# Performance work log

Hardware: AMD Instinct MI355X
Metric: run time of the kernel (lower is better)

Reference implementation:

```python
import jax, jax.numpy as jnp
import numpy as np
from jax import lax

T, B, XD, AD, H, OUT = 200, 1024, 48, 15, 512, 32
IN = XD + AD + 1  # 64


def _uniform(key, shape, scale):
    return jax.random.uniform(key, shape, jnp.float32, -scale, scale)


def setup_inputs() -> dict:
    key = jax.random.key(0)
    ks = jax.random.split(key, 16)
    k_lstm = 1.0 / np.sqrt(H)
    k1 = 1.0 / np.sqrt(H)
    k2 = 1.0 / np.sqrt(H + 1)
    return {
        "x": jax.random.normal(ks[0], (T, B, XD), jnp.float32),
        "a": jax.random.normal(ks[1], (T, B, AD), jnp.float32),
        "m": jax.random.uniform(ks[2], (T, B, 1), jnp.float32),
        # LSTM params (torch gate order: i, f, g, o)
        "w_ih": _uniform(ks[3], (4 * H, IN), k_lstm),
        "w_hh": _uniform(ks[4], (4 * H, H), k_lstm),
        "b_ih": _uniform(ks[5], (4 * H,), k_lstm),
        "b_hh": _uniform(ks[6], (4 * H,), k_lstm),
        # lin head: Linear(H, H+1) -> tanh -> Linear(H+1, OUT) -> tanh
        "lw1": _uniform(ks[7], (H + 1, H), k1),
        "lb1": _uniform(ks[8], (H + 1,), k1),
        "lw2": _uniform(ks[9], (OUT, H + 1), k2),
        "lb2": _uniform(ks[10], (OUT,), k2),
        # log_var head (same structure)
        "vw1": _uniform(ks[11], (H + 1, H), k1),
        "vb1": _uniform(ks[12], (H + 1,), k1),
        "vw2": _uniform(ks[13], (OUT, H + 1), k2),
        "vb2": _uniform(ks[14], (OUT,), k2),
    }


def _lstm(x_in, w_ih, w_hh, b_ih, b_hh):
    # x_in: [T, B, IN]; single-layer LSTM, zero initial state (torch default)
    b = x_in.shape[1]
    h0 = jnp.zeros((b, H), x_in.dtype)
    c0 = jnp.zeros((b, H), x_in.dtype)

    def step(carry, xt):
        h, c = carry
        gates = xt @ w_ih.T + b_ih + h @ w_hh.T + b_hh  # [B, 4H]
        i, f, g, o = jnp.split(gates, 4, axis=-1)
        c = jax.nn.sigmoid(f) * c + jax.nn.sigmoid(i) * jnp.tanh(g)
        h = jax.nn.sigmoid(o) * jnp.tanh(c)
        return (h, c), h

    _, hs = lax.scan(step, (h0, c0), x_in)
    return hs  # [T, B, H]


def _mlp(h, w1, b1, w2, b2):
    return jnp.tanh(jnp.tanh(h @ w1.T + b1) @ w2.T + b2)


def reference(x, a, m, w_ih, w_hh, b_ih, b_hh, lw1, lb1, lw2, lb2, vw1, vb1, vw2, vb2):
    # reverse=True
    x = jnp.flip(x, 0)
    a = jnp.flip(a, 0)
    m = jnp.flip(m, 0)
    t_steps = m.shape[0]
    t = jnp.arange(t_steps, dtype=x.dtype)[:, None, None] / jnp.max(m)  # [T,1,1]
    t = jnp.broadcast_to(t, (t_steps, m.shape[1], 1))
    x_in = jnp.concatenate([x, a, t], axis=-1)  # [T, B, IN]
    hs = _lstm(x_in, w_ih, w_hh, b_ih, b_hh)
    h_last = hs[-1]  # [B, H] (output_all=False)
    mu = _mlp(h_last, lw1, lb1, lw2, lb2)
    log_var = _mlp(h_last, vw1, vb1, vw2, vb2)
    return mu, log_var
```

## Files before the change

kernel.cpp:

```cpp
#include <hip/hip_runtime.h>
#include <cstdint>


typedef _Float16 f16;
typedef __attribute__((ext_vector_type(8))) _Float16 f16x8;
typedef __attribute__((ext_vector_type(8))) unsigned short u16x8;
typedef __attribute__((ext_vector_type(4))) float f32x4;

#define DEV __device__ __forceinline__

DEV float sigf(float x) { return 1.0f / (1.0f + expf(-x)); }

__global__ void __launch_bounds__(256)
wprep_kernel(const float* __restrict__ w_ih, const float* __restrict__ w_hh,
             uint4* __restrict__ wsw, unsigned* __restrict__ bar) {
  int idx = blockIdx.x * 256 + threadIdx.x;
  if (blockIdx.x == 0 && threadIdx.x < 256) bar[threadIdx.x] = 0u;
  if (idx >= 16 * 9 * 32 * 64) return;
  int jt = idx / 18432, rem = idx - jt * 18432;
  int ch = rem >> 11, r2 = rem & 2047;
  int Lb = r2 >> 6, lane = r2 & 63;
  int p = Lb & 1, ks = (Lb >> 1) & 1, jg = (Lb >> 2) & 1, g = Lb >> 3;
  int n = g * 512 + jt * 32 + jg * 16 + (lane & 15);
  int kb = ch * 64 + ks * 32 + (lane >> 4) * 8;
  f16x8 o;
#pragma unroll
  for (int e = 0; e < 8; e++) {
    int k = kb + e;
    float v = (k < 64) ? w_ih[n * 64 + k] : w_hh[(size_t)n * 512 + (k - 64)];
    f16 hi = (f16)v;
    o[e] = p ? (f16)(v - (float)hi) : hi;
  }
  wsw[idx] = *(uint4*)&o;
}

__global__ void __launch_bounds__(512, 2)
lstm_persist(const float* __restrict__ x, const float* __restrict__ a,
             const uint4* __restrict__ wsw,
             const float* __restrict__ b_ih, const float* __restrict__ b_hh,
             unsigned* __restrict__ hpk, float* __restrict__ h_final,
             const float* __restrict__ maxm_p, unsigned* __restrict__ bar) {
  __shared__ unsigned short sAB[2][24576];

  const int tid = threadIdx.x;
  const int lane = tid & 63;
  const int w = tid >> 6;
  const int rg = w >> 1, jg = w & 1;
  const int bid = blockIdx.x;
  const int mt = bid >> 4, jt = bid & 15;
  const int m0 = mt * 64;
  const int jjcol = jt * 32 + jg * 16 + (lane & 15);

  float bias[4];
#pragma unroll
  for (int g = 0; g < 4; g++)
    bias[g] = b_ih[g * 512 + jjcol] + b_hh[g * 512 + jjcol];
  f32x4 cc = {0.f, 0.f, 0.f, 0.f};
  const float mxm = *maxm_p;

  const int a_ln = tid & 63;
  const int a_La2 = tid >> 6;
  const int a_rg2 = a_La2 >> 1, a_ks2 = a_La2 & 1;
  const size_t a_off = (size_t)(m0 + a_rg2 * 16 + (a_ln & 15)) * 512 +
                       a_ks2 * 32 + (a_ln >> 4) * 8;

  for (int s = 0; s < 200; s++) {
    const int nch = (s == 0) ? 1 : 9;
    const int bin = s & 1;
    const unsigned* hin = hpk + (size_t)bin * 1024 * 512;
    unsigned* hout = hpk + (size_t)(bin ^ 1) * 1024 * 512;

    {
#pragma unroll
      for (int i = 0; i < 4; i++) {
        int id = tid + i * 512;
        uint4 v = wsw[(size_t)(jt * 9 + 0) * 2048 + id];
        *(uint4*)&sAB[0][8192 + id * 8] = v;
      }
      const float ts = (float)s / mxm;
      size_t srow = (size_t)(199 - s) * 1024 + m0;
      int row = tid >> 3, k8 = (tid & 7) * 8;
      float v[8];
#pragma unroll
      for (int e = 0; e < 8; e++) {
        int k = k8 + e;
        if (k < 48)      v[e] = x[(srow + row) * 48 + k];
        else if (k < 63) v[e] = a[(srow + row) * 15 + (k - 48)];
        else             v[e] = ts;
      }
      f16x8 hi, lo;
#pragma unroll
      for (int e = 0; e < 8; e++) {
        f16 h8 = (f16)v[e];
        hi[e] = h8; lo[e] = (f16)(v[e] - (float)h8);
      }
      int rg2 = row >> 4, ks2 = k8 >> 5;
      int ln = (((k8 & 31) >> 3) << 4) | (row & 15);
      int Lhi = (rg2 * 2 + ks2) * 2;
      *(f16x8*)&sAB[0][(Lhi * 64 + ln) * 8] = hi;
      *(f16x8*)&sAB[0][((Lhi + 1) * 64 + ln) * 8] = lo;
    }
    __syncthreads();

    f32x4 acc[4];
#pragma unroll
    for (int g = 0; g < 4; g++) acc[g] = (f32x4){0.f, 0.f, 0.f, 0.f};

    int cur = 0;
    for (int ch = 0; ch < nch; ch++) {
      const bool pref = (ch + 1 < nch);
      unsigned long long pa[4];
      uint4 pb[4];
      if (pref) {
        const unsigned* src = hin + a_off + ch * 64;
#pragma unroll
        for (int j = 0; j < 4; j++)
          pa[j] = __hip_atomic_load((const unsigned long long*)src + j,
                                    __ATOMIC_RELAXED, __HIP_MEMORY_SCOPE_AGENT);
#pragma unroll
        for (int i = 0; i < 4; i++)
          pb[i] = wsw[(size_t)(jt * 9 + ch + 1) * 2048 + tid + i * 512];
      }

      const unsigned short* buf = sAB[cur];
#pragma unroll
      for (int ks = 0; ks < 2; ks++) {
        f16x8 Ah = *(const f16x8*)&buf[(((rg * 2 + ks) * 2 + 0) * 64 + lane) * 8];
        f16x8 Al = *(const f16x8*)&buf[(((rg * 2 + ks) * 2 + 1) * 64 + lane) * 8];
        f16x8 Bh[4], Bl[4];
#pragma unroll
        for (int g = 0; g < 4; g++) {
          int base = 8192 + ((((g * 2 + jg) * 2 + ks) * 2) * 64 + lane) * 8;
          Bh[g] = *(const f16x8*)&buf[base];
          Bl[g] = *(const f16x8*)&buf[base + 512];
        }
        __builtin_amdgcn_s_setprio(1);
#pragma unroll
        for (int g = 0; g < 4; g++)
          acc[g] = __builtin_amdgcn_mfma_f32_16x16x32_f16(Ah, Bh[g], acc[g], 0, 0, 0);
#pragma unroll
        for (int g = 0; g < 4; g++)
          acc[g] = __builtin_amdgcn_mfma_f32_16x16x32_f16(Al, Bh[g], acc[g], 0, 0, 0);
#pragma unroll
        for (int g = 0; g < 4; g++)
          acc[g] = __builtin_amdgcn_mfma_f32_16x16x32_f16(Ah, Bl[g], acc[g], 0, 0, 0);
        __builtin_amdgcn_s_setprio(0);
      }

      if (pref) {
        unsigned short* nb = sAB[cur ^ 1];
        u16x8 HI, LO;
#pragma unroll
        for (int e = 0; e < 8; e++) {
          unsigned int u = (unsigned int)(pa[e >> 1] >> ((e & 1) * 32));
          HI[e] = (unsigned short)(u & 0xffffu);
          LO[e] = (unsigned short)(u >> 16);
        }
        int Lhi = a_La2 * 2;
        *(u16x8*)&nb[(Lhi * 64 + a_ln) * 8] = HI;
        *(u16x8*)&nb[((Lhi + 1) * 64 + a_ln) * 8] = LO;
#pragma unroll
        for (int i = 0; i < 4; i++)
          *(uint4*)&nb[8192 + (tid + i * 512) * 8] = pb[i];
      }
      __syncthreads();
      cur ^= 1;
    }

#pragma unroll
    for (int i = 0; i < 4; i++) {
      float gi = acc[0][i] + bias[0];
      float gf = acc[1][i] + bias[1];
      float gg = acc[2][i] + bias[2];
      float go = acc[3][i] + bias[3];
      float c = sigf(gf) * cc[i] + sigf(gi) * tanhf(gg);
      cc[i] = c;
      float h = sigf(go) * tanhf(c);
      size_t r = (size_t)(m0 + rg * 16 + (lane >> 4) * 4 + i) * 512 + jjcol;
      f16 h8 = (f16)h;
      f16 l8 = (f16)(h - (float)h8);
      unsigned pk = ((unsigned)__builtin_bit_cast(unsigned short, l8) << 16) |
                    (unsigned)__builtin_bit_cast(unsigned short, h8);
      __hip_atomic_store(&hout[r], pk, __ATOMIC_RELAXED, __HIP_MEMORY_SCOPE_AGENT);
      if (s == 199) h_final[r] = h;
    }

    __syncthreads();
    if (tid == 0) {
      __hip_atomic_fetch_add(&bar[mt * 16], 1u,
                             __ATOMIC_RELAXED, __HIP_MEMORY_SCOPE_AGENT);
      unsigned target = 16u * (unsigned)(s + 1);
      while (__hip_atomic_load(&bar[mt * 16], __ATOMIC_RELAXED,
                               __HIP_MEMORY_SCOPE_AGENT) < target)
        __builtin_amdgcn_s_sleep(2);
    }
    __syncthreads();
  }
}

__global__ void __launch_bounds__(1024)
maxm_kernel(const float* __restrict__ mv, float* __restrict__ out) {
  __shared__ float red[1024];
  int tid = threadIdx.x;
  float mx = -3.0e38f;
  for (int i = tid; i < 200 * 1024; i += 1024) mx = fmaxf(mx, mv[i]);
  red[tid] = mx;
  __syncthreads();
  for (int s = 512; s > 0; s >>= 1) {
    if (tid < s) red[tid] = fmaxf(red[tid], red[tid + s]);
    __syncthreads();
  }
  if (tid == 0) *out = red[0];
}

__global__ void __launch_bounds__(256, 2)
head1_valu(const float* __restrict__ h, const float* __restrict__ lw1,
           const float* __restrict__ lb1, const float* __restrict__ vw1,
           const float* __restrict__ vb1, float* __restrict__ z) {
  __shared__ float sAT[64 * 68];
  const int tid = threadIdx.x;
  const int rg = tid & 15;
  const int cgrp = tid >> 4;
  const int bid = blockIdx.x;
  const int mt = bid & 15, nt = bid >> 4;
  const int m0 = mt * 64;
  const int nb = nt * 64 + cgrp * 4;

  const float* wr[4];
  float bias[4];
  int hdv[4], wnv[4], valid[4];
#pragma unroll
  for (int c = 0; c < 4; c++) {
    int n = nb + c;
    valid[c] = (n < 1026);
    int hd = valid[c] ? (n >= 513) : 0;
    int wn = valid[c] ? (n - hd * 513) : 0;
    hdv[c] = hd; wnv[c] = wn;
    wr[c] = (hd ? vw1 : lw1) + (size_t)wn * 512;
    bias[c] = valid[c] ? (hd ? vb1[wn] : lb1[wn]) : 0.f;
  }

  float acc[4][4];
#pragma unroll
  for (int i = 0; i < 4; i++)
#pragma unroll
    for (int c = 0; c < 4; c++) acc[i][c] = 0.f;

  for (int ch = 0; ch < 8; ch++) {
    int k0 = ch * 64;
    for (int idx = tid; idx < 4096; idx += 256) {
      int row = idx >> 6, k = idx & 63;
      sAT[k * 68 + row] = h[(size_t)(m0 + row) * 512 + k0 + k];
    }
    __syncthreads();
#pragma unroll 4
    for (int k4 = 0; k4 < 16; k4++) {
      f32x4 wv[4];
#pragma unroll
      for (int c = 0; c < 4; c++)
        wv[c] = *(const f32x4*)(wr[c] + k0 + k4 * 4);
      f32x4 rv[4];
#pragma unroll
      for (int kk = 0; kk < 4; kk++)
        rv[kk] = *(const f32x4*)&sAT[(k4 * 4 + kk) * 68 + rg * 4];
#pragma unroll
      for (int kk = 0; kk < 4; kk++)
#pragma unroll
        for (int c = 0; c < 4; c++) {
          acc[0][c] += rv[kk][0] * wv[c][kk];
          acc[1][c] += rv[kk][1] * wv[c][kk];
          acc[2][c] += rv[kk][2] * wv[c][kk];
          acc[3][c] += rv[kk][3] * wv[c][kk];
        }
    }
    __syncthreads();
  }
#pragma unroll
  for (int c = 0; c < 4; c++) {
    if (!valid[c]) continue;
#pragma unroll
    for (int i = 0; i < 4; i++) {
      int m = m0 + rg * 4 + i;
      z[(size_t)hdv[c] * 1024 * 520 + (size_t)m * 520 + wnv[c]] =
          tanhf(acc[i][c] + bias[c]);
    }
  }
}

__global__ void __launch_bounds__(256)
head2_valu(const float* __restrict__ z, const float* __restrict__ lw2,
           const float* __restrict__ lb2, const float* __restrict__ vw2,
           const float* __restrict__ vb2, float* __restrict__ out) {
  __shared__ float sZ[8 * 133];
  __shared__ float sW[32 * 133];
  const int tid = threadIdx.x;
  const int bid = blockIdx.x;
  const int gr0 = bid * 8;
  const int hd = gr0 >> 10;
  const int b0 = gr0 & 1023;
  const float* w2 = hd ? vw2 : lw2;
  const float* b2 = hd ? vb2 : lb2;
  const float* zh = z + (size_t)hd * 1024 * 520;
  const int rloc = tid >> 5, col = tid & 31;
  float acc = 0.f;

  for (int ch = 0; ch < 5; ch++) {
    int kc = ch * 128;
    for (int idx = tid; idx < 1024; idx += 256) {
      int row = idx >> 7, k = idx & 127;
      int kk = kc + k;
      sZ[row * 133 + k] = (kk < 513) ? zh[(size_t)(b0 + row) * 520 + kk] : 0.f;
    }
    for (int idx = tid; idx < 4096; idx += 256) {
      int row = idx >> 7, k = idx & 127;
      int kk = kc + k;
      sW[row * 133 + k] = (kk < 513) ? w2[(size_t)row * 513 + kk] : 0.f;
    }
    __syncthreads();
#pragma unroll 8
    for (int k = 0; k < 128; k++)
      acc += sZ[rloc * 133 + k] * sW[col * 133 + k];
    __syncthreads();
  }
  out[(size_t)hd * 32768 + (size_t)(b0 + rloc) * 32 + col] = tanhf(acc + b2[col]);
}

extern "C" void kernel_launch(void* const* d_in, const int* in_sizes, int n_in,
                              void* d_out, int out_size, void* d_ws, size_t ws_size,
                              hipStream_t stream) {
  (void)in_sizes; (void)n_in; (void)out_size; (void)ws_size;
  const float* x    = (const float*)d_in[0];
  const float* a    = (const float*)d_in[1];
  const float* mm   = (const float*)d_in[2];
  const float* w_ih = (const float*)d_in[3];
  const float* w_hh = (const float*)d_in[4];
  const float* b_ih = (const float*)d_in[5];
  const float* b_hh = (const float*)d_in[6];
  const float* lw1  = (const float*)d_in[7];
  const float* lb1  = (const float*)d_in[8];
  const float* lw2  = (const float*)d_in[9];
  const float* lb2  = (const float*)d_in[10];
  const float* vw1  = (const float*)d_in[11];
  const float* vb1  = (const float*)d_in[12];
  const float* vw2  = (const float*)d_in[13];
  const float* vb2  = (const float*)d_in[14];

  char* wsb = (char*)d_ws;
  float*    maxm  = (float*)wsb;
  unsigned* bar   = (unsigned*)(wsb + 256);
  float*    z     = (float*)(wsb + 4096);
  float*    h_fin = (float*)(wsb + 4263936);
  uint4*    wsw   = (uint4*)(wsb + 6361088);
  unsigned* hpk   = (unsigned*)(wsb + 11079680);

  maxm_kernel<<<1, 1024, 0, stream>>>(mm, maxm);
  wprep_kernel<<<1152, 256, 0, stream>>>(w_ih, w_hh, wsw, bar);

  {
    const float* xa = x; const float* aa = a;
    const uint4* wswa = wsw;
    const float* biha = b_ih; const float* bhha = b_hh;
    unsigned* hpka = hpk;
    float* hfa = h_fin; const float* mxa = maxm;
    unsigned* bara = bar;
    void* kargs[] = {&xa, &aa, &wswa, &biha, &bhha,
                     &hpka, &hfa, &mxa, &bara};
    hipLaunchCooperativeKernel((void*)lstm_persist, dim3(256), dim3(512),
                               kargs, 0, stream);
  }

  head1_valu<<<272, 256, 0, stream>>>(h_fin, lw1, lb1, vw1, vb1, z);
  head2_valu<<<256, 256, 0, stream>>>(z, lw2, lb2, vw2, vb2, (float*)d_out);
}
```

Measured before the change: 4.754 ms.

## Prefetch next-step inputs before barrier and deepen chunk prefetch to two stages

Loads the next timestep's x/a inputs and the first weight chunk into registers before the inter-block barrier spin, so they no longer sit on the critical path at the start of each step. The chunk loop is fully unrolled with a two-deep register prefetch of h and weight chunks instead of one-deep. Nontemporal hints are added for streamed inputs and the final output. This raises register pressure, which could lower occupancy or cause spills.

```diff
diff --git a/kernel.cpp b/kernel.cpp
--- a/kernel.cpp
+++ b/kernel.cpp
@@ -64,41 +64,49 @@
   const size_t a_off = (size_t)(m0 + a_rg2 * 16 + (a_ln & 15)) * 512 +
                        a_ks2 * 32 + (a_ln >> 4) * 8;
 
+  const int xs_row = tid >> 3, xs_k8 = (tid & 7) * 8;
+  const int xs_rg2 = xs_row >> 4, xs_ks2 = xs_k8 >> 5;
+  const int xs_ln = (((xs_k8 & 31) >> 3) << 4) | (xs_row & 15);
+  const int xs_Lhi = (xs_rg2 * 2 + xs_ks2) * 2;
+
+  float xv[8];
+  uint4 b0r[4];
+  {
+    size_t srow = (size_t)199 * 1024 + m0;
+#pragma unroll
+    for (int e = 0; e < 8; e++) {
+      int k = xs_k8 + e;
+      if (k < 48)
+        xv[e] = __builtin_nontemporal_load(&x[(srow + xs_row) * 48 + k]);
+      else if (k < 63)
+        xv[e] = __builtin_nontemporal_load(&a[(srow + xs_row) * 15 + (k - 48)]);
+      else
+        xv[e] = 0.f;
+    }
+#pragma unroll
+    for (int i = 0; i < 4; i++)
+      b0r[i] = wsw[(size_t)(jt * 9) * 2048 + tid + i * 512];
+  }
+
   for (int s = 0; s < 200; s++) {
-    const int nch = (s == 0) ? 1 : 9;
     const int bin = s & 1;
     const unsigned* hin = hpk + (size_t)bin * 1024 * 512;
     unsigned* hout = hpk + (size_t)(bin ^ 1) * 1024 * 512;
 
     {
-#pragma unroll
-      for (int i = 0; i < 4; i++) {
-        int id = tid + i * 512;
-        uint4 v = wsw[(size_t)(jt * 9 + 0) * 2048 + id];
-        *(uint4*)&sAB[0][8192 + id * 8] = v;
+      const float ts = (float)s / mxm;
+      f16x8 hi, lo;
+#pragma unroll
+      for (int e = 0; e < 8; e++) {
+        float v = (xs_k8 + e == 63) ? ts : xv[e];
+        f16 h8 = (f16)v;
+        hi[e] = h8; lo[e] = (f16)(v - (float)h8);
       }
-      const float ts = (float)s / mxm;
-      size_t srow = (size_t)(199 - s) * 1024 + m0;
-      int row = tid >> 3, k8 = (tid & 7) * 8;
-      float v[8];
-#pragma unroll
-      for (int e = 0; e < 8; e++) {
-        int k = k8 + e;
-        if (k < 48)      v[e] = x[(srow + row) * 48 + k];
-        else if (k < 63) v[e] = a[(srow + row) * 15 + (k - 48)];
-        else             v[e] = ts;
-      }
-      f16x8 hi, lo;
-#pragma unroll
-      for (int e = 0; e < 8; e++) {
-        f16 h8 = (f16)v[e];
-        hi[e] = h8; lo[e] = (f16)(v[e] - (float)h8);
-      }
-      int rg2 = row >> 4, ks2 = k8 >> 5;
-      int ln = (((k8 & 31) >> 3) << 4) | (row & 15);
-      int Lhi = (rg2 * 2 + ks2) * 2;
-      *(f16x8*)&sAB[0][(Lhi * 64 + ln) * 8] = hi;
-      *(f16x8*)&sAB[0][((Lhi + 1) * 64 + ln) * 8] = lo;
+      *(f16x8*)&sAB[0][(xs_Lhi * 64 + xs_ln) * 8] = hi;
+      *(f16x8*)&sAB[0][((xs_Lhi + 1) * 64 + xs_ln) * 8] = lo;
+#pragma unroll
+      for (int i = 0; i < 4; i++)
+        *(uint4*)&sAB[0][8192 + (tid + i * 512) * 8] = b0r[i];
     }
     __syncthreads();
 
@@ -106,23 +114,7 @@
 #pragma unroll
     for (int g = 0; g < 4; g++) acc[g] = (f32x4){0.f, 0.f, 0.f, 0.f};
 
-    int cur = 0;
-    for (int ch = 0; ch < nch; ch++) {
-      const bool pref = (ch + 1 < nch);
-      unsigned long long pa[4];
-      uint4 pb[4];
-      if (pref) {
-        const unsigned* src = hin + a_off + ch * 64;
-#pragma unroll
-        for (int j = 0; j < 4; j++)
-          pa[j] = __hip_atomic_load((const unsigned long long*)src + j,
-                                    __ATOMIC_RELAXED, __HIP_MEMORY_SCOPE_AGENT);
-#pragma unroll
-        for (int i = 0; i < 4; i++)
-          pb[i] = wsw[(size_t)(jt * 9 + ch + 1) * 2048 + tid + i * 512];
-      }
-
-      const unsigned short* buf = sAB[cur];
+    auto mfma_chunk = [&](const unsigned short* buf) {
 #pragma unroll
       for (int ks = 0; ks < 2; ks++) {
         f16x8 Ah = *(const f16x8*)&buf[(((rg * 2 + ks) * 2 + 0) * 64 + lane) * 8];
@@ -146,25 +138,56 @@
           acc[g] = __builtin_amdgcn_mfma_f32_16x16x32_f16(Ah, Bl[g], acc[g], 0, 0, 0);
         __builtin_amdgcn_s_setprio(0);
       }
-
-      if (pref) {
-        unsigned short* nb = sAB[cur ^ 1];
-        u16x8 HI, LO;
-#pragma unroll
-        for (int e = 0; e < 8; e++) {
-          unsigned int u = (unsigned int)(pa[e >> 1] >> ((e & 1) * 32));
-          HI[e] = (unsigned short)(u & 0xffffu);
-          LO[e] = (unsigned short)(u >> 16);
+    };
+    auto issue_A = [&](int c, unsigned long long* dst) {
+      const unsigned* src = hin + a_off + (size_t)(c - 1) * 64;
+#pragma unroll
+      for (int j = 0; j < 4; j++)
+        dst[j] = __hip_atomic_load((const unsigned long long*)src + j,
+                                   __ATOMIC_RELAXED, __HIP_MEMORY_SCOPE_AGENT);
+    };
+    auto issue_B = [&](int c, uint4* dst) {
+#pragma unroll
+      for (int i = 0; i < 4; i++)
+        dst[i] = wsw[(size_t)(jt * 9 + c) * 2048 + tid + i * 512];
+    };
+    auto write_stage = [&](const unsigned long long* pa_, const uint4* pb_,
+                           unsigned short* nb) {
+      u16x8 HI, LO;
+#pragma unroll
+      for (int e = 0; e < 8; e++) {
+        unsigned u = (unsigned)(pa_[e >> 1] >> ((e & 1) * 32));
+        HI[e] = (unsigned short)(u & 0xffffu);
+        LO[e] = (unsigned short)(u >> 16);
+      }
+      int Lhi = a_La2 * 2;
+      *(u16x8*)&nb[(Lhi * 64 + a_ln) * 8] = HI;
+      *(u16x8*)&nb[((Lhi + 1) * 64 + a_ln) * 8] = LO;
+#pragma unroll
+      for (int i = 0; i < 4; i++)
+        *(uint4*)&nb[8192 + (tid + i * 512) * 8] = pb_[i];
+    };
+
+    if (s == 0) {
+      mfma_chunk(sAB[0]);
+    } else {
+      unsigned long long pa[2][4];
+      uint4 pb[2][4];
+      issue_A(1, pa[1]); issue_B(1, pb[1]);
+      issue_A(2, pa[0]); issue_B(2, pb[0]);
+#pragma unroll
+      for (int ch = 0; ch < 9; ch++) {
+        mfma_chunk(sAB[ch & 1]);
+        if (ch < 8) {
+          write_stage(pa[(ch + 1) & 1], pb[(ch + 1) & 1],
+                      (unsigned short*)sAB[(ch + 1) & 1]);
+          if (ch + 3 <= 8) {
+            issue_A(ch + 3, pa[(ch + 3) & 1]);
+            issue_B(ch + 3, pb[(ch + 3) & 1]);
+          }
+          __syncthreads();
         }
-        int Lhi = a_La2 * 2;
-        *(u16x8*)&nb[(Lhi * 64 + a_ln) * 8] = HI;
-        *(u16x8*)&nb[((Lhi + 1) * 64 + a_ln) * 8] = LO;
-#pragma unroll
-        for (int i = 0; i < 4; i++)
-          *(uint4*)&nb[8192 + (tid + i * 512) * 8] = pb[i];
       }
-      __syncthreads();
-      cur ^= 1;
     }
 
 #pragma unroll
@@ -182,7 +205,22 @@
       unsigned pk = ((unsigned)__builtin_bit_cast(unsigned short, l8) << 16) |
                     (unsigned)__builtin_bit_cast(unsigned short, h8);
       __hip_atomic_store(&hout[r], pk, __ATOMIC_RELAXED, __HIP_MEMORY_SCOPE_AGENT);
-      if (s == 199) h_final[r] = h;
+      if (s == 199) __builtin_nontemporal_store(h, &h_final[r]);
+    }
+
+    if (s < 199) {
+      size_t srow = (size_t)(198 - s) * 1024 + m0;
+#pragma unroll
+      for (int e = 0; e < 8; e++) {
+        int k = xs_k8 + e;
+        if (k < 48)
+          xv[e] = __builtin_nontemporal_load(&x[(srow + xs_row) * 48 + k]);
+        else if (k < 63)
+          xv[e] = __builtin_nontemporal_load(&a[(srow + xs_row) * 15 + (k - 48)]);
+      }
+#pragma unroll
+      for (int i = 0; i < 4; i++)
+        b0r[i] = wsw[(size_t)(jt * 9) * 2048 + tid + i * 512];
     }
 
     __syncthreads();
```

Result: slower. 5.201 ms (+9.4%).
